# Optimization experiments

Hardware: AMD Instinct MI355X
Metric: run time of the kernel (lower is better)

Reference implementation:

```python
import jax, jax.numpy as jnp
import numpy as np

# Mamba3/SSD selective state-space mixer (scalar-A-per-head SSD recurrence,
# causal depthwise conv on x/B/C, gated RMSNorm, in/out projections).
D_MODEL = 1024
EXPAND = 2
D_INNER = EXPAND * D_MODEL            # 2048
HEADDIM = D_MODEL // 16               # 64  (head_count=16 -> headdim 64)
NHEADS = D_INNER // HEADDIM           # 32
D_STATE = 128
CONV_W = 4
CONV_DIM = D_INNER + 2 * D_STATE      # x, B, C share the conv
D_IN_PROJ = 2 * D_INNER + 2 * D_STATE + NHEADS  # z, x, B, C, dt
EPS = 1e-5


def setup_inputs() -> dict:
    key = jax.random.key(0)
    ks = jax.random.split(key, 8)
    B, L = 4, 2048
    hidden = jax.random.normal(ks[0], (B, L, D_MODEL), dtype=jnp.float32)
    W_in = jax.random.normal(ks[1], (D_MODEL, D_IN_PROJ), dtype=jnp.float32) * 0.02
    conv_w = jax.random.normal(ks[2], (CONV_DIM, CONV_W), dtype=jnp.float32) * 0.2
    conv_b = jnp.zeros((CONV_DIM,), dtype=jnp.float32)
    # dt_bias: inverse-softplus of dt ~ U[1e-3, 0.1]
    dt = jnp.exp(jax.random.uniform(ks[3], (NHEADS,)) * (np.log(0.1) - np.log(1e-3)) + np.log(1e-3))
    dt_bias = dt + jnp.log(-jnp.expm1(-dt))
    A_log = jnp.log(jax.random.uniform(ks[4], (NHEADS,), minval=1.0, maxval=16.0))
    D = jnp.ones((NHEADS,), dtype=jnp.float32)
    norm_w = jnp.ones((D_INNER,), dtype=jnp.float32)
    W_out = jax.random.normal(ks[5], (D_INNER, D_MODEL), dtype=jnp.float32) * 0.02
    return {"hidden": hidden, "W_in": W_in, "conv_w": conv_w, "conv_b": conv_b,
            "dt_bias": dt_bias, "A_log": A_log, "D": D, "norm_w": norm_w, "W_out": W_out}


def _silu(x):
    return x * jax.nn.sigmoid(x)


def _mixer(hidden, W_in, conv_w, conv_b, dt_bias, A_log, D, norm_w, W_out):
    Bsz, L, _ = hidden.shape
    zxbcdt = hidden @ W_in                                    # [B,L,D_IN_PROJ]
    z = zxbcdt[..., :D_INNER]
    xBC = zxbcdt[..., D_INNER:D_INNER + CONV_DIM]
    dt = zxbcdt[..., -NHEADS:]                                # [B,L,H]
    # causal depthwise conv, width 4 (small fixed loop over taps)
    xp = jnp.pad(xBC, ((0, 0), (CONV_W - 1, 0), (0, 0)))
    conv = sum(xp[:, k:k + L, :] * conv_w[:, k] for k in range(CONV_W))
    xBC = _silu(conv + conv_b)
    x = xBC[..., :D_INNER].reshape(Bsz, L, NHEADS, HEADDIM)   # [B,L,H,P]
    Bm = xBC[..., D_INNER:D_INNER + D_STATE]                  # [B,L,N]
    Cm = xBC[..., D_INNER + D_STATE:]                         # [B,L,N]
    dt = jax.nn.softplus(dt + dt_bias)                        # [B,L,H]
    dA = jnp.exp(dt * (-jnp.exp(A_log)))                      # [B,L,H] decay in (0,1)
    dBx = jnp.einsum('blh,bln,blhp->blhpn', dt, Bm, x)        # [B,L,H,P,N]

    def step(h, inp):
        dA_t, dBx_t, C_t = inp                                # [B,H],[B,H,P,N],[B,N]
        h = dA_t[:, :, None, None] * h + dBx_t
        y = jnp.einsum('bhpn,bn->bhp', h, C_t)
        return h, y

    h0 = jnp.zeros((Bsz, NHEADS, HEADDIM, D_STATE), dtype=hidden.dtype)
    xs = (jnp.moveaxis(dA, 1, 0), jnp.moveaxis(dBx, 1, 0), jnp.moveaxis(Cm, 1, 0))
    _, ys = jax.lax.scan(step, h0, xs)                        # [L,B,H,P]
    y = jnp.moveaxis(ys, 0, 1) + D[None, None, :, None] * x   # skip term
    y = y.reshape(Bsz, L, D_INNER)
    # gated RMSNorm: norm(y * silu(z))
    y = y * _silu(z)
    y = y * jax.lax.rsqrt(jnp.mean(y * y, axis=-1, keepdims=True) + EPS) * norm_w
    return y @ W_out


def reference(hidden, W_in, conv_w, conv_b, dt_bias, A_log, D, norm_w, W_out):
    return _mixer(hidden, W_in, conv_w, conv_b, dt_bias, A_log, D, norm_w, W_out)
```

## Files before the change

kernel.cpp:

```cpp
#include <hip/hip_runtime.h>
#include <math.h>

#define BSZ 4
#define LEN 2048
#define DM 1024
#define DI 2048
#define HD 64
#define NH 32
#define DS 128
#define CD 2304
#define DP 4384
#define NTOK (BSZ*LEN)
#define QCH 128
#define NCH (LEN/QCH)
#define TOFF (DP-NH)

#define CONV_R 64
#define NRB (NTOK/CONV_R)
#define NPAD 4480
#define GLD 136

typedef unsigned short ushort_t;
typedef __bf16 bf16x8 __attribute__((ext_vector_type(8)));
typedef ushort_t us8 __attribute__((ext_vector_type(8)));
typedef float f32x4 __attribute__((ext_vector_type(4)));

__device__ __forceinline__ ushort_t f2bf(float f) {
    unsigned u = __float_as_uint(f);
    unsigned r = (u + 0x7FFFu + ((u >> 16) & 1u)) >> 16;
    return (ushort_t)r;
}
__device__ __forceinline__ float bf2f(ushort_t u) {
    return __uint_as_float(((unsigned)u) << 16);
}
__device__ __forceinline__ bf16x8 us2bf(us8 v) {
    union { us8 u; bf16x8 b; } x; x.u = v; return x.b;
}

__device__ __forceinline__ void gl_lds16(const void* g, void* l) {
    __builtin_amdgcn_global_load_lds(
        (const __attribute__((address_space(1))) void*)g,
        (__attribute__((address_space(3))) void*)l, 16, 0, 0);
}

__global__ __launch_bounds__(256) void cvt_bf16(
    const float* __restrict__ A, ushort_t* __restrict__ Ab)
{
    size_t i = ((size_t)blockIdx.x * 256 + threadIdx.x) * 4;
    float4 v = *(const float4*)(A + i);
    ushort_t o[4] = { f2bf(v.x), f2bf(v.y), f2bf(v.z), f2bf(v.w) };
    *(uint2*)(Ab + i) = *(uint2*)o;
}

__global__ __launch_bounds__(256) void transpose_cvt(
    const float* __restrict__ W, ushort_t* __restrict__ Wt,
    int K, int N, int ldw)
{
    __shared__ float T[32][33];
    const int n0 = blockIdx.x * 32;
    const int k0 = blockIdx.y * 32;
    const int tid = threadIdx.x;
    #pragma unroll
    for (int l = 0; l < 4; l++) {
        int idx = tid + l * 256;
        int ki = idx >> 5, nj = idx & 31;
        int n = n0 + nj;
        T[ki][nj] = (n < N) ? W[(size_t)(k0 + ki) * ldw + n] : 0.f;
    }
    __syncthreads();
    #pragma unroll
    for (int l = 0; l < 4; l++) {
        int idx = tid + l * 256;
        int nj = idx >> 5, ki = idx & 31;
        Wt[(size_t)(n0 + nj) * K + k0 + ki] = f2bf(T[ki][nj]);
    }
}

template <bool OB>
__global__ __launch_bounds__(256) void gemm_bf16(
    const ushort_t* __restrict__ A, const ushort_t* __restrict__ Bt,
    void* __restrict__ Cp, int K, int lda, int ldb, int ldc, int nmax)
{
    __shared__ __align__(16) ushort_t As[128 * 32];
    __shared__ __align__(16) ushort_t Bs[128 * 32];
    const int tid = threadIdx.x;
    const int n0 = blockIdx.x * 128;
    const int m0 = blockIdx.y * 128;
    const int lane = tid & 63;
    const int w = tid >> 6;
    const int wm = w >> 1, wn = w & 1;
    const int lm = lane & 15, quad = lane >> 4;

    const int srow = tid >> 2;
    const int skq = (tid & 3) * 8;
    const ushort_t* ga0 = A + (size_t)(m0 + srow) * lda + skq;
    const ushort_t* ga1 = A + (size_t)(m0 + 64 + srow) * lda + skq;
    const ushort_t* gb0 = Bt + (size_t)(n0 + srow) * ldb + skq;
    const ushort_t* gb1 = Bt + (size_t)(n0 + 64 + srow) * ldb + skq;
    ushort_t* la0 = &As[srow * 32 + skq];
    ushort_t* la1 = &As[(64 + srow) * 32 + skq];
    ushort_t* lb0 = &Bs[srow * 32 + skq];
    ushort_t* lb1 = &Bs[(64 + srow) * 32 + skq];

    f32x4 acc[4][4];
    #pragma unroll
    for (int i = 0; i < 4; i++)
        #pragma unroll
        for (int j = 0; j < 4; j++) acc[i][j] = (f32x4){0.f, 0.f, 0.f, 0.f};

    for (int k0 = 0; k0 < K; k0 += 32) {
        gl_lds16(ga0, la0);
        gl_lds16(ga1, la1);
        gl_lds16(gb0, lb0);
        gl_lds16(gb1, lb1);
        ga0 += 32; ga1 += 32; gb0 += 32; gb1 += 32;
        __syncthreads();
        bf16x8 af[4], bfr[4];
        #pragma unroll
        for (int i = 0; i < 4; i++)
            af[i] = *(const bf16x8*)&As[(wm * 64 + i * 16 + lm) * 32 + quad * 8];
        #pragma unroll
        for (int j = 0; j < 4; j++)
            bfr[j] = *(const bf16x8*)&Bs[(wn * 64 + j * 16 + lm) * 32 + quad * 8];
        #pragma unroll
        for (int i = 0; i < 4; i++)
            #pragma unroll
            for (int j = 0; j < 4; j++)
                acc[i][j] = __builtin_amdgcn_mfma_f32_16x16x32_bf16(af[i], bfr[j], acc[i][j], 0, 0, 0);
        __syncthreads();
    }

    #pragma unroll
    for (int i = 0; i < 4; i++) {
        int row = m0 + wm * 64 + i * 16 + quad * 4;
        #pragma unroll
        for (int j = 0; j < 4; j++) {
            int col = n0 + wn * 64 + j * 16 + lm;
            if (col < nmax) {
                #pragma unroll
                for (int r = 0; r < 4; r++) {
                    if (OB)
                        ((ushort_t*)Cp)[(size_t)(row + r) * ldc + col] = f2bf(acc[i][j][r]);
                    else
                        ((float*)Cp)[(size_t)(row + r) * ldc + col] = acc[i][j][r];
                }
            }
        }
    }
}

__global__ __launch_bounds__(256) void conv_silu_bf16(
    const ushort_t* __restrict__ xbcb, const float* __restrict__ cw,
    const float* __restrict__ cb, ushort_t* __restrict__ xT,
    ushort_t* __restrict__ Bn, ushort_t* __restrict__ BT,
    ushort_t* __restrict__ Cn)
{
    __shared__ ushort_t Tl[256][68];
    const int tid = threadIdx.x;
    const int c = blockIdx.x * 256 + tid;
    const int rb = blockIdx.y;
    const int row0 = rb * CONV_R;
    const bool isBC = (blockIdx.x == 8);

    const float w0 = cw[c*4+0], w1 = cw[c*4+1], w2 = cw[c*4+2], w3 = cw[c*4+3];
    const float bias = cb[c];
    float h0 = 0.f, h1 = 0.f, h2 = 0.f;
    if ((row0 & (LEN - 1)) != 0) {
        h0 = bf2f(xbcb[(size_t)(row0 - 3) * CD + c]);
        h1 = bf2f(xbcb[(size_t)(row0 - 2) * CD + c]);
        h2 = bf2f(xbcb[(size_t)(row0 - 1) * CD + c]);
    }
    const ushort_t* p = xbcb + (size_t)row0 * CD + c;
    for (int r = 0; r < CONV_R; r++) {
        float xin = bf2f(*p);
        float a = bias + w0*h0 + w1*h1 + w2*h2 + w3*xin;
        ushort_t bv = f2bf(a / (1.f + __expf(-a)));
        Tl[tid][r] = bv;
        if (isBC) {
            int row = row0 + r;
            if (tid < DS) Bn[(size_t)row * DS + tid] = bv;
            else          Cn[(size_t)row * DS + (tid - DS)] = bv;
        }
        h0 = h1; h1 = h2; h2 = xin;
        p += CD;
    }
    __syncthreads();

    const int seg = tid & 7;
    const int clb = tid >> 3;
    if (!isBC) {
        #pragma unroll
        for (int pass = 0; pass < 8; pass++) {
            int cl = pass * 32 + clb;
            int cc = blockIdx.x * 256 + cl;
            us8 v;
            #pragma unroll
            for (int j = 0; j < 8; j++) v[j] = Tl[cl][seg * 8 + j];
            *(us8*)&xT[(size_t)cc * NTOK + row0 + seg * 8] = v;
        }
    } else {
        #pragma unroll
        for (int pass = 0; pass < 4; pass++) {
            int n = pass * 32 + clb;
            us8 v;
            #pragma unroll
            for (int j = 0; j < 8; j++) v[j] = Tl[n][seg * 8 + j];
            *(us8*)&BT[(size_t)n * NTOK + row0 + seg * 8] = v;
        }
    }
}

__global__ __launch_bounds__(256) void dt_proc_fp32(
    const float* __restrict__ hidden, const float* __restrict__ W_in,
    const float* __restrict__ dt_bias, const float* __restrict__ A_log,
    float* __restrict__ dtv, float* __restrict__ ldA)
{
    const int h = threadIdx.x & 31;
    const int tt = threadIdx.x >> 5;
    const int t = blockIdx.x * 8 + tt;
    const float* hr = hidden + (size_t)t * DM;
    const float* wc = W_in + TOFF + h;
    float a0 = 0.f, a1 = 0.f, a2 = 0.f, a3 = 0.f;
    for (int k = 0; k < DM; k += 4) {
        a0 += hr[k+0] * wc[(size_t)(k+0) * DP];
        a1 += hr[k+1] * wc[(size_t)(k+1) * DP];
        a2 += hr[k+2] * wc[(size_t)(k+2) * DP];
        a3 += hr[k+3] * wc[(size_t)(k+3) * DP];
    }
    float v = (a0 + a1) + (a2 + a3) + dt_bias[h];
    float sp = (v > 20.f) ? v : log1pf(expf(v));
    int idx = t * NH + h;
    dtv[idx] = sp;
    ldA[idx] = -sp * expf(A_log[h]);
}

__global__ __launch_bounds__(64) void scan_chunk(
    const float* __restrict__ dtv, const float* __restrict__ ldA,
    float* __restrict__ lcpb, float* __restrict__ dtsb,
    float* __restrict__ coefb, float* __restrict__ csum)
{
    const int blk = blockIdx.x;
    const int chunk = blk % NCH;
    const int bh = blk / NCH;
    const int h = bh % NH;
    const int b = bh / NH;
    const int lane = threadIdx.x;
    const size_t rowbase = (size_t)b * LEN + (size_t)chunk * QCH;
    const int t0 = 2 * lane, t1 = 2 * lane + 1;
    float v0 = ldA[(rowbase + t0) * NH + h];
    float v1 = ldA[(rowbase + t1) * NH + h];
    float d0 = dtv[(rowbase + t0) * NH + h];
    float d1 = dtv[(rowbase + t1) * NH + h];
    float pair = v0 + v1;
    #pragma unroll
    for (int off = 1; off < 64; off <<= 1) {
        float n = __shfl_up(pair, off, 64);
        if (lane >= off) pair += n;
    }
    float l1 = pair, l0 = pair - v1;
    float total = __shfl(pair, 63, 64);
    size_t base = (size_t)blk * QCH;
    *(float2*)&lcpb[base + t0] = make_float2(l0, l1);
    *(float2*)&dtsb[base + t0] = make_float2(d0, d1);
    *(float2*)&coefb[base + t0] =
        make_float2(__expf(total - l0) * d0, __expf(total - l1) * d1);
    if (lane == 63) csum[blk] = total;
}

__global__ __launch_bounds__(256) void phase1_mfma(
    const ushort_t* __restrict__ xT, const ushort_t* __restrict__ BT,
    const float* __restrict__ coefb, float* __restrict__ S)
{
    const int blk = blockIdx.x;
    const int chunk = blk % NCH;
    const int bh = blk / NCH;
    const int h = bh % NH;
    const int b = bh / NH;
    const int tid = threadIdx.x;
    const size_t rowbase = (size_t)b * LEN + (size_t)chunk * QCH;

    __shared__ float coef[QCH];
    if (tid < QCH) coef[tid] = coefb[(size_t)blk * QCH + tid];
    __syncthreads();

    const int w = tid >> 6, lane = tid & 63;
    const int lm = lane & 15, quad = lane >> 4;
    const int nw0 = w * 32;

    f32x4 acc[4][2];
    #pragma unroll
    for (int i = 0; i < 4; i++)
        #pragma unroll
        for (int j = 0; j < 2; j++) acc[i][j] = (f32x4){0.f, 0.f, 0.f, 0.f};

    #pragma unroll
    for (int ks = 0; ks < 4; ks++) {
        const int k0 = ks * 32 + quad * 8;
        bf16x8 a[4];
        #pragma unroll
        for (int mi = 0; mi < 4; mi++)
            a[mi] = *(const bf16x8*)&xT[(size_t)(h * HD + mi * 16 + lm) * NTOK + rowbase + k0];
        float cf[8];
        #pragma unroll
        for (int j = 0; j < 8; j++) cf[j] = coef[k0 + j];
        #pragma unroll
        for (int ni = 0; ni < 2; ni++) {
            us8 raw = *(const us8*)&BT[(size_t)(nw0 + ni * 16 + lm) * NTOK + rowbase + k0];
            us8 sb;
            #pragma unroll
            for (int j = 0; j < 8; j++) sb[j] = f2bf(bf2f(raw[j]) * cf[j]);
            bf16x8 bfr = us2bf(sb);
            #pragma unroll
            for (int mi = 0; mi < 4; mi++)
                acc[mi][ni] = __builtin_amdgcn_mfma_f32_16x16x32_bf16(a[mi], bfr, acc[mi][ni], 0, 0, 0);
        }
    }
    float* Sb = S + (size_t)blk * (HD * DS);
    #pragma unroll
    for (int mi = 0; mi < 4; mi++)
        #pragma unroll
        for (int ni = 0; ni < 2; ni++)
            #pragma unroll
            for (int r = 0; r < 4; r++)
                Sb[(size_t)(mi * 16 + quad * 4 + r) * DS + nw0 + ni * 16 + lm] = acc[mi][ni][r];
}

__global__ __launch_bounds__(256) void phase2(
    const float* __restrict__ S, const float* __restrict__ csum,
    ushort_t* __restrict__ hsb)
{
    const int bh = blockIdx.x >> 3;
    const int esl = blockIdx.x & 7;
    const int tid = threadIdx.x;
    const int eb = esl * 1024 + tid;
    float run[4] = {0.f, 0.f, 0.f, 0.f};
    for (int c = 0; c < NCH; c++) {
        float P = __expf(csum[bh * NCH + c]);
        size_t base = (size_t)(bh * NCH + c) * (HD * DS);
        #pragma unroll
        for (int i = 0; i < 4; i++) {
            size_t idx = base + eb + i * 256;
            float s = S[idx];
            hsb[idx] = f2bf(run[i]);
            run[i] = P * run[i] + s;
        }
    }
}

__global__ __launch_bounds__(256) void phase3_mfma(
    const ushort_t* __restrict__ xT, const ushort_t* __restrict__ Bn,
    const ushort_t* __restrict__ Cn, const ushort_t* __restrict__ hsb,
    const float* __restrict__ lcpb, const float* __restrict__ dtsb,
    const float* __restrict__ Dvec, ushort_t* __restrict__ ybuf)
{
    const int tid = threadIdx.x;
    const int blk = blockIdx.x;
    const int chunk = blk % NCH;
    const int bh = blk / NCH;
    const int h = bh % NH;
    const int b = bh / NH;
    const size_t rowbase = (size_t)b * LEN + (size_t)chunk * QCH;

    __shared__ float lcp[QCH];
    __shared__ float dts[QCH];
    __shared__ __align__(16) ushort_t Gs[QCH * GLD];

    if (tid < QCH) {
        lcp[tid] = lcpb[(size_t)blk * QCH + tid];
        dts[tid] = dtsb[(size_t)blk * QCH + tid];
    }
    __syncthreads();

    const int w = tid >> 6, lane = tid & 63;
    const int lm = lane & 15, quad = lane >> 4;

    {
        const int sw0 = w * 32;
        f32x4 acc[2][8];
        #pragma unroll
        for (int si = 0; si < 2; si++)
            #pragma unroll
            for (int ti = 0; ti < 8; ti++) acc[si][ti] = (f32x4){0.f, 0.f, 0.f, 0.f};

        #pragma unroll
        for (int ks = 0; ks < 4; ks++) {
            const int k0 = ks * 32 + quad * 8;
            bf16x8 a0 = *(const bf16x8*)&Bn[(rowbase + sw0 + lm) * DS + k0];
            bf16x8 a1 = *(const bf16x8*)&Bn[(rowbase + sw0 + 16 + lm) * DS + k0];
            #pragma unroll
            for (int ti = 0; ti < 8; ti++) {
                bf16x8 cf = *(const bf16x8*)&Cn[(rowbase + ti * 16 + lm) * DS + k0];
                acc[0][ti] = __builtin_amdgcn_mfma_f32_16x16x32_bf16(a0, cf, acc[0][ti], 0, 0, 0);
                acc[1][ti] = __builtin_amdgcn_mfma_f32_16x16x32_bf16(a1, cf, acc[1][ti], 0, 0, 0);
            }
        }
        #pragma unroll
        for (int si = 0; si < 2; si++)
            #pragma unroll
            for (int ti = 0; ti < 8; ti++) {
                int t = ti * 16 + lm;
                float lt = lcp[t];
                ushort_t pk[4];
                #pragma unroll
                for (int r = 0; r < 4; r++) {
                    int s = sw0 + si * 16 + quad * 4 + r;
                    float wv = (s <= t) ? (__expf(lt - lcp[s]) * dts[s]) : 0.f;
                    pk[r] = f2bf(acc[si][ti][r] * wv);
                }
                *(ushort4*)&Gs[t * GLD + sw0 + si * 16 + quad * 4] = *(ushort4*)pk;
            }
    }
    __syncthreads();

    const int tw0 = w * 32;
    const ushort_t* hsb_ = hsb + (size_t)blk * (HD * DS);
    f32x4 acc2[2][4];
    #pragma unroll
    for (int ti = 0; ti < 2; ti++)
        #pragma unroll
        for (int pi = 0; pi < 4; pi++) acc2[ti][pi] = (f32x4){0.f, 0.f, 0.f, 0.f};

    #pragma unroll
    for (int ks = 0; ks < 8; ks++) {
        bf16x8 a[2], bb[4];
        if (ks < 4) {
            const int k0 = ks * 32 + quad * 8;
            a[0] = *(const bf16x8*)&Gs[(tw0 + lm) * GLD + k0];
            a[1] = *(const bf16x8*)&Gs[(tw0 + 16 + lm) * GLD + k0];
            #pragma unroll
            for (int pi = 0; pi < 4; pi++)
                bb[pi] = *(const bf16x8*)&xT[(size_t)(h * HD + pi * 16 + lm) * NTOK + rowbase + k0];
        } else {
            const int k0 = (ks - 4) * 32 + quad * 8;
            #pragma unroll
            for (int ti = 0; ti < 2; ti++) {
                int t = tw0 + ti * 16 + lm;
                float sc = __expf(lcp[t]);
                us8 raw = *(const us8*)&Cn[(rowbase + t) * DS + k0];
                us8 sb;
                #pragma unroll
                for (int j = 0; j < 8; j++) sb[j] = f2bf(bf2f(raw[j]) * sc);
                a[ti] = us2bf(sb);
            }
            #pragma unroll
            for (int pi = 0; pi < 4; pi++)
                bb[pi] = *(const bf16x8*)&hsb_[(size_t)(pi * 16 + lm) * DS + k0];
        }
        #pragma unroll
        for (int ti = 0; ti < 2; ti++)
            #pragma unroll
            for (int pi = 0; pi < 4; pi++)
                acc2[ti][pi] = __builtin_amdgcn_mfma_f32_16x16x32_bf16(a[ti], bb[pi], acc2[ti][pi], 0, 0, 0);
    }

    const float Dh = Dvec[h];
    ushort_t* yb = ybuf + (size_t)blk * (HD * QCH);
    #pragma unroll
    for (int ti = 0; ti < 2; ti++)
        #pragma unroll
        for (int pi = 0; pi < 4; pi++) {
            int tb = tw0 + ti * 16 + quad * 4;
            ushort4 xv = *(const ushort4*)&xT[(size_t)(h * HD + pi * 16 + lm) * NTOK + rowbase + tb];
            const ushort_t* xe = (const ushort_t*)&xv;
            #pragma unroll
            for (int r = 0; r < 4; r++) {
                float y = acc2[ti][pi][r] + Dh * bf2f(xe[r]);
                yb[(size_t)(tb + r) * HD + pi * 16 + lm] = f2bf(y);
            }
        }
}

__global__ __launch_bounds__(256) void gate_rms(
    const ushort_t* __restrict__ zb, const ushort_t* __restrict__ ybuf,
    const float* __restrict__ nw, ushort_t* __restrict__ ynb)
{
    const int row = blockIdx.x;
    const int tid = threadIdx.x;
    const int b = row >> 11;
    const int l = row & (LEN - 1);
    const int chunk = l >> 7;
    const int t = l & (QCH - 1);
    const ushort_t* zr = zb + (size_t)row * DI;
    float g[8];
    float ss = 0.f;
    #pragma unroll
    for (int i = 0; i < 8; i++) {
        int c = tid + i * 256;
        int h = c >> 6;
        int p = c & 63;
        float y = bf2f(ybuf[((size_t)((b * NH + h) * NCH + chunk)) * (HD * QCH) + t * HD + p]);
        float z = bf2f(zr[c]);
        float sg = z / (1.f + __expf(-z));
        float v = y * sg;
        g[i] = v;
        ss += v * v;
    }
    #pragma unroll
    for (int off = 32; off > 0; off >>= 1) ss += __shfl_down(ss, off, 64);
    __shared__ float red[4];
    if ((tid & 63) == 0) red[tid >> 6] = ss;
    __syncthreads();
    float tot = red[0] + red[1] + red[2] + red[3];
    float r = rsqrtf(tot * (1.f / DI) + 1e-5f);
    #pragma unroll
    for (int i = 0; i < 8; i++) {
        int c = tid + i * 256;
        ynb[(size_t)row * DI + c] = f2bf(g[i] * r * nw[c]);
    }
}

extern "C" void kernel_launch(void* const* d_in, const int* in_sizes, int n_in,
                              void* d_out, int out_size, void* d_ws, size_t ws_size,
                              hipStream_t stream)
{
    const float* hidden  = (const float*)d_in[0];
    const float* W_in    = (const float*)d_in[1];
    const float* conv_w  = (const float*)d_in[2];
    const float* conv_b  = (const float*)d_in[3];
    const float* dt_bias = (const float*)d_in[4];
    const float* A_log   = (const float*)d_in[5];
    const float* Dv      = (const float*)d_in[6];
    const float* norm_w  = (const float*)d_in[7];
    const float* W_out   = (const float*)d_in[8];
    float* out = (float*)d_out;

    char* ws = (char*)d_ws;
    size_t o = 0;
    ushort_t* zb   = (ushort_t*)(ws + o); o += (size_t)NTOK * DI * 2;
    ushort_t* xbcb = (ushort_t*)(ws + o); o += (size_t)NTOK * CD * 2;
    float* S       = (float*)(ws + o);    o += (size_t)BSZ * NH * NCH * HD * DS * 4;
    ushort_t* xT   = (ushort_t*)(ws + o); o += (size_t)DI * NTOK * 2;
    ushort_t* Bn   = (ushort_t*)(ws + o); o += (size_t)NTOK * DS * 2;
    ushort_t* BT   = (ushort_t*)(ws + o); o += (size_t)DS * NTOK * 2;
    ushort_t* Cn   = (ushort_t*)(ws + o); o += (size_t)NTOK * DS * 2;
    ushort_t* hsb  = (ushort_t*)(ws + o); o += (size_t)BSZ * NH * NCH * HD * DS * 2;
    float* dtv     = (float*)(ws + o);    o += (size_t)NTOK * NH * 4;
    float* ldA     = (float*)(ws + o);    o += (size_t)NTOK * NH * 4;
    float* lcpb    = (float*)(ws + o);    o += (size_t)BSZ * NH * LEN * 4;
    float* dtsb    = (float*)(ws + o);    o += (size_t)BSZ * NH * LEN * 4;
    float* coefb   = (float*)(ws + o);    o += (size_t)BSZ * NH * LEN * 4;
    float* csum    = (float*)(ws + o);    o += (size_t)BSZ * NH * NCH * 4;
    ushort_t* Ah   = (ushort_t*)S;
    ushort_t* W1t  = (ushort_t*)((char*)S + (size_t)NTOK * DM * 2);
    ushort_t* ybuf = (ushort_t*)S;
    ushort_t* Wot  = hsb;
    ushort_t* ynb  = xbcb;

    cvt_bf16<<<(NTOK * DM) / 1024, 256, 0, stream>>>(hidden, Ah);
    transpose_cvt<<<dim3(NPAD / 32, DM / 32), 256, 0, stream>>>(W_in, W1t, DM, DP, DP);
    gemm_bf16<true><<<dim3(DI / 128, NTOK / 128), 256, 0, stream>>>(
        Ah, W1t, zb, DM, DM, DM, DI, DI);
    gemm_bf16<true><<<dim3(19, NTOK / 128), 256, 0, stream>>>(
        Ah, W1t + (size_t)DI * DM, xbcb, DM, DM, DM, CD, CD);
    conv_silu_bf16<<<dim3(CD / 256, NRB), 256, 0, stream>>>(
        xbcb, conv_w, conv_b, xT, Bn, BT, Cn);
    dt_proc_fp32<<<NTOK / 8, 256, 0, stream>>>(hidden, W_in, dt_bias, A_log, dtv, ldA);
    scan_chunk<<<BSZ * NH * NCH, 64, 0, stream>>>(dtv, ldA, lcpb, dtsb, coefb, csum);
    phase1_mfma<<<BSZ * NH * NCH, 256, 0, stream>>>(xT, BT, coefb, S);
    phase2<<<BSZ * NH * 8, 256, 0, stream>>>(S, csum, hsb);
    phase3_mfma<<<BSZ * NH * NCH, 256, 0, stream>>>(
        xT, Bn, Cn, hsb, lcpb, dtsb, Dv, ybuf);
    gate_rms<<<NTOK, 256, 0, stream>>>(zb, ybuf, norm_w, ynb);
    transpose_cvt<<<dim3(DM / 32, DI / 32), 256, 0, stream>>>(W_out, Wot, DI, DM, DM);
    gemm_bf16<false><<<dim3(DM / 128, NTOK / 128), 256, 0, stream>>>(
        ynb, Wot, out, DI, DI, DI, DM, DM);
}
```

Baseline: 577.5 us.

## Share C·Bᵀ Gram across heads, merge in-proj GEMMs, reorder chunk blocks

Computes the per-chunk C·Bᵀ Gram matrix once per (batch, chunk) in a new kernel and reuses it across all 32 heads in phase3, where every head previously recomputed it. The two input-projection GEMMs become one GEMM over the padded width, writing z and xBC into a single strided buffer. Phase1 and phase3 block indices now place the head innermost so neighbouring blocks share chunk data in cache. The cost is an extra fp32 Gram buffer that phase3 reads from global memory and masks per element, plus a wider padded output for the fused GEMM.

```diff
diff --git a/kernel.cpp b/kernel.cpp
--- a/kernel.cpp
+++ b/kernel.cpp
@@ -18,7 +18,6 @@
 #define CONV_R 64
 #define NRB (NTOK/CONV_R)
 #define NPAD 4480
-#define GLD 136
 
 typedef unsigned short ushort_t;
 typedef __bf16 bf16x8 __attribute__((ext_vector_type(8)));
@@ -166,11 +165,11 @@
     const float bias = cb[c];
     float h0 = 0.f, h1 = 0.f, h2 = 0.f;
     if ((row0 & (LEN - 1)) != 0) {
-        h0 = bf2f(xbcb[(size_t)(row0 - 3) * CD + c]);
-        h1 = bf2f(xbcb[(size_t)(row0 - 2) * CD + c]);
-        h2 = bf2f(xbcb[(size_t)(row0 - 1) * CD + c]);
-    }
-    const ushort_t* p = xbcb + (size_t)row0 * CD + c;
+        h0 = bf2f(xbcb[(size_t)(row0 - 3) * NPAD + c]);
+        h1 = bf2f(xbcb[(size_t)(row0 - 2) * NPAD + c]);
+        h2 = bf2f(xbcb[(size_t)(row0 - 1) * NPAD + c]);
+    }
+    const ushort_t* p = xbcb + (size_t)row0 * NPAD + c;
     for (int r = 0; r < CONV_R; r++) {
         float xin = bf2f(*p);
         float a = bias + w0*h0 + w1*h1 + w2*h2 + w3*xin;
@@ -182,7 +181,7 @@
             else          Cn[(size_t)row * DS + (tid - DS)] = bv;
         }
         h0 = h1; h1 = h2; h2 = xin;
-        p += CD;
+        p += NPAD;
     }
     __syncthreads();
 
@@ -208,6 +207,47 @@
             *(us8*)&BT[(size_t)n * NTOK + row0 + seg * 8] = v;
         }
     }
+}
+
+__global__ __launch_bounds__(256) void gct_gemm(
+    const ushort_t* __restrict__ Bn, const ushort_t* __restrict__ Cn,
+    float* __restrict__ Graw)
+{
+    const int bc = blockIdx.x;
+    const int chunk = bc % NCH;
+    const int b = bc / NCH;
+    const size_t rowbase = (size_t)b * LEN + (size_t)chunk * QCH;
+    const int tid = threadIdx.x;
+    const int w = tid >> 6, lane = tid & 63;
+    const int lm = lane & 15, quad = lane >> 4;
+    const int tw0 = w * 32;
+
+    f32x4 acc[2][8];
+    #pragma unroll
+    for (int ti = 0; ti < 2; ti++)
+        #pragma unroll
+        for (int sj = 0; sj < 8; sj++) acc[ti][sj] = (f32x4){0.f, 0.f, 0.f, 0.f};
+
+    #pragma unroll
+    for (int ks = 0; ks < 4; ks++) {
+        const int k0 = ks * 32 + quad * 8;
+        bf16x8 a0 = *(const bf16x8*)&Cn[(rowbase + tw0 + lm) * DS + k0];
+        bf16x8 a1 = *(const bf16x8*)&Cn[(rowbase + tw0 + 16 + lm) * DS + k0];
+        #pragma unroll
+        for (int sj = 0; sj < 8; sj++) {
+            bf16x8 bb = *(const bf16x8*)&Bn[(rowbase + sj * 16 + lm) * DS + k0];
+            acc[0][sj] = __builtin_amdgcn_mfma_f32_16x16x32_bf16(a0, bb, acc[0][sj], 0, 0, 0);
+            acc[1][sj] = __builtin_amdgcn_mfma_f32_16x16x32_bf16(a1, bb, acc[1][sj], 0, 0, 0);
+        }
+    }
+    float* G = Graw + (size_t)bc * (QCH * QCH);
+    #pragma unroll
+    for (int ti = 0; ti < 2; ti++)
+        #pragma unroll
+        for (int sj = 0; sj < 8; sj++)
+            #pragma unroll
+            for (int r = 0; r < 4; r++)
+                G[(size_t)(tw0 + ti * 16 + quad * 4 + r) * QCH + sj * 16 + lm] = acc[ti][sj][r];
 }
 
 __global__ __launch_bounds__(256) void dt_proc_fp32(
@@ -271,16 +311,16 @@
     const ushort_t* __restrict__ xT, const ushort_t* __restrict__ BT,
     const float* __restrict__ coefb, float* __restrict__ S)
 {
-    const int blk = blockIdx.x;
-    const int chunk = blk % NCH;
-    const int bh = blk / NCH;
-    const int h = bh % NH;
-    const int b = bh / NH;
+    const int h = blockIdx.x & (NH - 1);
+    const int bc = blockIdx.x >> 5;
+    const int chunk = bc % NCH;
+    const int b = bc / NCH;
+    const int blko = (b * NH + h) * NCH + chunk;
     const int tid = threadIdx.x;
     const size_t rowbase = (size_t)b * LEN + (size_t)chunk * QCH;
 
     __shared__ float coef[QCH];
-    if (tid < QCH) coef[tid] = coefb[(size_t)blk * QCH + tid];
+    if (tid < QCH) coef[tid] = coefb[(size_t)blko * QCH + tid];
     __syncthreads();
 
     const int w = tid >> 6, lane = tid & 63;
@@ -315,7 +355,7 @@
                 acc[mi][ni] = __builtin_amdgcn_mfma_f32_16x16x32_bf16(a[mi], bfr, acc[mi][ni], 0, 0, 0);
         }
     }
-    float* Sb = S + (size_t)blk * (HD * DS);
+    float* Sb = S + (size_t)blko * (HD * DS);
     #pragma unroll
     for (int mi = 0; mi < 4; mi++)
         #pragma unroll
@@ -348,72 +388,34 @@
 }
 
 __global__ __launch_bounds__(256) void phase3_mfma(
-    const ushort_t* __restrict__ xT, const ushort_t* __restrict__ Bn,
-    const ushort_t* __restrict__ Cn, const ushort_t* __restrict__ hsb,
+    const ushort_t* __restrict__ xT, const ushort_t* __restrict__ Cn,
+    const ushort_t* __restrict__ hsb, const float* __restrict__ Graw,
     const float* __restrict__ lcpb, const float* __restrict__ dtsb,
     const float* __restrict__ Dvec, ushort_t* __restrict__ ybuf)
 {
     const int tid = threadIdx.x;
-    const int blk = blockIdx.x;
-    const int chunk = blk % NCH;
-    const int bh = blk / NCH;
-    const int h = bh % NH;
-    const int b = bh / NH;
+    const int h = blockIdx.x & (NH - 1);
+    const int bc = blockIdx.x >> 5;
+    const int chunk = bc % NCH;
+    const int b = bc / NCH;
+    const int blko = (b * NH + h) * NCH + chunk;
     const size_t rowbase = (size_t)b * LEN + (size_t)chunk * QCH;
 
     __shared__ float lcp[QCH];
     __shared__ float dts[QCH];
-    __shared__ __align__(16) ushort_t Gs[QCH * GLD];
-
     if (tid < QCH) {
-        lcp[tid] = lcpb[(size_t)blk * QCH + tid];
-        dts[tid] = dtsb[(size_t)blk * QCH + tid];
+        lcp[tid] = lcpb[(size_t)blko * QCH + tid];
+        dts[tid] = dtsb[(size_t)blko * QCH + tid];
     }
     __syncthreads();
 
     const int w = tid >> 6, lane = tid & 63;
     const int lm = lane & 15, quad = lane >> 4;
-
-    {
-        const int sw0 = w * 32;
-        f32x4 acc[2][8];
-        #pragma unroll
-        for (int si = 0; si < 2; si++)
-            #pragma unroll
-            for (int ti = 0; ti < 8; ti++) acc[si][ti] = (f32x4){0.f, 0.f, 0.f, 0.f};
-
-        #pragma unroll
-        for (int ks = 0; ks < 4; ks++) {
-            const int k0 = ks * 32 + quad * 8;
-            bf16x8 a0 = *(const bf16x8*)&Bn[(rowbase + sw0 + lm) * DS + k0];
-            bf16x8 a1 = *(const bf16x8*)&Bn[(rowbase + sw0 + 16 + lm) * DS + k0];
-            #pragma unroll
-            for (int ti = 0; ti < 8; ti++) {
-                bf16x8 cf = *(const bf16x8*)&Cn[(rowbase + ti * 16 + lm) * DS + k0];
-                acc[0][ti] = __builtin_amdgcn_mfma_f32_16x16x32_bf16(a0, cf, acc[0][ti], 0, 0, 0);
-                acc[1][ti] = __builtin_amdgcn_mfma_f32_16x16x32_bf16(a1, cf, acc[1][ti], 0, 0, 0);
-            }
-        }
-        #pragma unroll
-        for (int si = 0; si < 2; si++)
-            #pragma unroll
-            for (int ti = 0; ti < 8; ti++) {
-                int t = ti * 16 + lm;
-                float lt = lcp[t];
-                ushort_t pk[4];
-                #pragma unroll
-                for (int r = 0; r < 4; r++) {
-                    int s = sw0 + si * 16 + quad * 4 + r;
-                    float wv = (s <= t) ? (__expf(lt - lcp[s]) * dts[s]) : 0.f;
-                    pk[r] = f2bf(acc[si][ti][r] * wv);
-                }
-                *(ushort4*)&Gs[t * GLD + sw0 + si * 16 + quad * 4] = *(ushort4*)pk;
-            }
-    }
-    __syncthreads();
-
     const int tw0 = w * 32;
-    const ushort_t* hsb_ = hsb + (size_t)blk * (HD * DS);
+
+    const float* Gr = Graw + (size_t)bc * (QCH * QCH);
+    const ushort_t* hsp = hsb + (size_t)blko * (HD * DS);
+
     f32x4 acc2[2][4];
     #pragma unroll
     for (int ti = 0; ti < 2; ti++)
@@ -425,8 +427,23 @@
         bf16x8 a[2], bb[4];
         if (ks < 4) {
             const int k0 = ks * 32 + quad * 8;
-            a[0] = *(const bf16x8*)&Gs[(tw0 + lm) * GLD + k0];
-            a[1] = *(const bf16x8*)&Gs[(tw0 + 16 + lm) * GLD + k0];
+            #pragma unroll
+            for (int ti = 0; ti < 2; ti++) {
+                int t = tw0 + ti * 16 + lm;
+                float lt = lcp[t];
+                const float* gp = Gr + (size_t)t * QCH + k0;
+                float4 g0 = *(const float4*)gp;
+                float4 g1 = *(const float4*)(gp + 4);
+                float ge[8] = { g0.x, g0.y, g0.z, g0.w, g1.x, g1.y, g1.z, g1.w };
+                us8 sb;
+                #pragma unroll
+                for (int j = 0; j < 8; j++) {
+                    int s = k0 + j;
+                    float wv = (s <= t) ? (__expf(lt - lcp[s]) * dts[s]) : 0.f;
+                    sb[j] = f2bf(ge[j] * wv);
+                }
+                a[ti] = us2bf(sb);
+            }
             #pragma unroll
             for (int pi = 0; pi < 4; pi++)
                 bb[pi] = *(const bf16x8*)&xT[(size_t)(h * HD + pi * 16 + lm) * NTOK + rowbase + k0];
@@ -444,7 +461,7 @@
             }
             #pragma unroll
             for (int pi = 0; pi < 4; pi++)
-                bb[pi] = *(const bf16x8*)&hsb_[(size_t)(pi * 16 + lm) * DS + k0];
+                bb[pi] = *(const bf16x8*)&hsp[(size_t)(pi * 16 + lm) * DS + k0];
         }
         #pragma unroll
         for (int ti = 0; ti < 2; ti++)
@@ -454,7 +471,7 @@
     }
 
     const float Dh = Dvec[h];
-    ushort_t* yb = ybuf + (size_t)blk * (HD * QCH);
+    ushort_t* yb = ybuf + (size_t)blko * (HD * QCH);
     #pragma unroll
     for (int ti = 0; ti < 2; ti++)
         #pragma unroll
@@ -471,8 +488,8 @@
 }
 
 __global__ __launch_bounds__(256) void gate_rms(
-    const ushort_t* __restrict__ zb, const ushort_t* __restrict__ ybuf,
-    const float* __restrict__ nw, ushort_t* __restrict__ ynb)
+    ushort_t* __restrict__ zxb, const ushort_t* __restrict__ ybuf,
+    const float* __restrict__ nw)
 {
     const int row = blockIdx.x;
     const int tid = threadIdx.x;
@@ -480,7 +497,7 @@
     const int l = row & (LEN - 1);
     const int chunk = l >> 7;
     const int t = l & (QCH - 1);
-    const ushort_t* zr = zb + (size_t)row * DI;
+    ushort_t* zr = zxb + (size_t)row * NPAD;
     float g[8];
     float ss = 0.f;
     #pragma unroll
@@ -505,7 +522,7 @@
     #pragma unroll
     for (int i = 0; i < 8; i++) {
         int c = tid + i * 256;
-        ynb[(size_t)row * DI + c] = f2bf(g[i] * r * nw[c]);
+        zr[DI + c] = f2bf(g[i] * r * nw[c]);
     }
 }
 
@@ -526,14 +543,14 @@
 
     char* ws = (char*)d_ws;
     size_t o = 0;
-    ushort_t* zb   = (ushort_t*)(ws + o); o += (size_t)NTOK * DI * 2;
-    ushort_t* xbcb = (ushort_t*)(ws + o); o += (size_t)NTOK * CD * 2;
+    ushort_t* zxb  = (ushort_t*)(ws + o); o += (size_t)NTOK * NPAD * 2;
     float* S       = (float*)(ws + o);    o += (size_t)BSZ * NH * NCH * HD * DS * 4;
     ushort_t* xT   = (ushort_t*)(ws + o); o += (size_t)DI * NTOK * 2;
     ushort_t* Bn   = (ushort_t*)(ws + o); o += (size_t)NTOK * DS * 2;
     ushort_t* BT   = (ushort_t*)(ws + o); o += (size_t)DS * NTOK * 2;
     ushort_t* Cn   = (ushort_t*)(ws + o); o += (size_t)NTOK * DS * 2;
     ushort_t* hsb  = (ushort_t*)(ws + o); o += (size_t)BSZ * NH * NCH * HD * DS * 2;
+    float* Graw    = (float*)(ws + o);    o += (size_t)BSZ * NCH * QCH * QCH * 4;
     float* dtv     = (float*)(ws + o);    o += (size_t)NTOK * NH * 4;
     float* ldA     = (float*)(ws + o);    o += (size_t)NTOK * NH * 4;
     float* lcpb    = (float*)(ws + o);    o += (size_t)BSZ * NH * LEN * 4;
@@ -544,24 +561,24 @@
     ushort_t* W1t  = (ushort_t*)((char*)S + (size_t)NTOK * DM * 2);
     ushort_t* ybuf = (ushort_t*)S;
     ushort_t* Wot  = hsb;
-    ushort_t* ynb  = xbcb;
+    ushort_t* xbcb = zxb + DI;
+    ushort_t* ynb  = zxb + DI;
 
     cvt_bf16<<<(NTOK * DM) / 1024, 256, 0, stream>>>(hidden, Ah);
     transpose_cvt<<<dim3(NPAD / 32, DM / 32), 256, 0, stream>>>(W_in, W1t, DM, DP, DP);
-    gemm_bf16<true><<<dim3(DI / 128, NTOK / 128), 256, 0, stream>>>(
-        Ah, W1t, zb, DM, DM, DM, DI, DI);
-    gemm_bf16<true><<<dim3(19, NTOK / 128), 256, 0, stream>>>(
-        Ah, W1t + (size_t)DI * DM, xbcb, DM, DM, DM, CD, CD);
+    gemm_bf16<true><<<dim3(NPAD / 128, NTOK / 128), 256, 0, stream>>>(
+        Ah, W1t, zxb, DM, DM, DM, NPAD, NPAD);
     conv_silu_bf16<<<dim3(CD / 256, NRB), 256, 0, stream>>>(
         xbcb, conv_w, conv_b, xT, Bn, BT, Cn);
+    gct_gemm<<<BSZ * NCH, 256, 0, stream>>>(Bn, Cn, Graw);
     dt_proc_fp32<<<NTOK / 8, 256, 0, stream>>>(hidden, W_in, dt_bias, A_log, dtv, ldA);
     scan_chunk<<<BSZ * NH * NCH, 64, 0, stream>>>(dtv, ldA, lcpb, dtsb, coefb, csum);
     phase1_mfma<<<BSZ * NH * NCH, 256, 0, stream>>>(xT, BT, coefb, S);
     phase2<<<BSZ * NH * 8, 256, 0, stream>>>(S, csum, hsb);
     phase3_mfma<<<BSZ * NH * NCH, 256, 0, stream>>>(
-        xT, Bn, Cn, hsb, lcpb, dtsb, Dv, ybuf);
-    gate_rms<<<NTOK, 256, 0, stream>>>(zb, ybuf, norm_w, ynb);
+        xT, Cn, hsb, Graw, lcpb, dtsb, Dv, ybuf);
+    gate_rms<<<NTOK, 256, 0, stream>>>(zxb, ybuf, norm_w);
     transpose_cvt<<<dim3(DM / 32, DI / 32), 256, 0, stream>>>(W_out, Wot, DI, DM, DM);
     gemm_bf16<false><<<dim3(DM / 128, NTOK / 128), 256, 0, stream>>>(
-        ynb, Wot, out, DI, DI, DI, DM, DM);
-}
+        ynb, Wot, out, DI, NPAD, DI, DM, DM);
+}
```

Result: faster. 539.7 us (-6.5%).
